# Optimization experiments

Hardware: AMD Instinct MI355X
Metric: run time of the kernel (lower is better)

The kernel has to match this reference:

```python
import jax, jax.numpy as jnp
import numpy as np

# SMPL/STAR kinematic tree: parent of joint i (i = 1..23)
PARENT = np.array([0, 0, 0, 1, 2, 3, 4, 5, 6, 7, 8, 9, 9, 9, 12, 13, 14, 16, 17, 18, 19, 20, 21])
B, V, J, NB = 512, 6890, 24, 10


def _axis_angle_parts(theta):
    # theta: [N,3] axis-angle. Matches STAR: norm of (theta + 1e-8).
    angle = jnp.linalg.norm(theta + 1e-8, axis=1, keepdims=True)  # [N,1]
    normalized = theta / angle
    half = angle * 0.5
    return jnp.cos(half), jnp.sin(half), normalized


def quat_feat(theta):
    c, s, n = _axis_angle_parts(theta)
    return jnp.concatenate([s * n, c - 1.0], axis=1)  # [N,4]


def rodrigues(theta):
    c, s, n = _axis_angle_parts(theta)
    w = c[:, 0]
    xyz = s * n
    x, y, z = xyz[:, 0], xyz[:, 1], xyz[:, 2]
    xx, yy, zz = x * x, y * y, z * z
    wx, wy, wz = w * x, w * y, w * z
    xy, xz, yz = x * y, x * z, y * z
    R = jnp.stack([
        1 - 2 * (yy + zz), 2 * (xy - wz), 2 * (xz + wy),
        2 * (xy + wz), 1 - 2 * (xx + zz), 2 * (yz - wx),
        2 * (xz - wy), 2 * (yz + wx), 1 - 2 * (xx + yy)], axis=-1)
    return R.reshape(-1, 3, 3)


def setup_inputs() -> dict:
    key = jax.random.key(0)
    ks = jax.random.split(key, 8)
    pose = jax.random.normal(ks[0], (B, 72), jnp.float32)
    betas = jax.random.normal(ks[1], (B, NB), jnp.float32)
    trans = jax.random.normal(ks[2], (B, 3), jnp.float32)
    v_template = jax.random.normal(ks[3], (V, 3), jnp.float32)
    shapedirs = jax.random.normal(ks[4], (V * 3, NB), jnp.float32) * 0.01
    posedirs = jax.random.normal(ks[5], (V * 3, 93), jnp.float32) * 0.01
    J_regressor = jax.random.uniform(ks[6], (J, V), jnp.float32)
    J_regressor = J_regressor / jnp.sum(J_regressor, axis=1, keepdims=True)
    weights = jax.random.uniform(ks[7], (V, J), jnp.float32)
    weights = weights / jnp.sum(weights, axis=1, keepdims=True)
    return {"pose": pose, "betas": betas, "trans": trans,
            "v_template": v_template, "shapedirs": shapedirs,
            "posedirs": posedirs, "J_regressor": J_regressor,
            "weights": weights}


def reference(pose, betas, trans, v_template, shapedirs, posedirs, J_regressor, weights):
    b = pose.shape[0]
    # shape blendshapes
    v_shaped = jnp.einsum('dk,bk->bd', shapedirs, betas).reshape(b, V, 3) + v_template[None]
    Jp = jnp.einsum('bik,ji->bjk', v_shaped, J_regressor)
    # pose features: quat feats of joints 1..23 + second beta
    pose_quat = quat_feat(pose.reshape(-1, 3)).reshape(b, -1)   # [b,96]
    pose_feat = jnp.concatenate([pose_quat[:, 4:], betas[:, 1:2]], axis=1)  # [b,93]
    R = rodrigues(pose.reshape(-1, 3)).reshape(b, J, 3, 3)
    # pose blendshapes
    v_posed = v_shaped + jnp.einsum('dk,bk->bd', posedirs, pose_feat).reshape(b, V, 3)
    # relative joint locations
    J_rel = jnp.concatenate([Jp[:, :1], Jp[:, 1:] - Jp[:, PARENT]], axis=1)  # [b,24,3]
    # local transforms [b,24,4,4]
    G_local = jnp.concatenate([R, J_rel[:, :, :, None]], axis=-1)
    pad = jnp.broadcast_to(jnp.array([0., 0., 0., 1.], jnp.float32).reshape(1, 1, 1, 4), (b, J, 1, 4))
    G_local = jnp.concatenate([G_local, pad], axis=2)
    # serial forward kinematics (fixed 24-joint chain)
    Gs = [G_local[:, 0]]
    for i in range(1, J):
        Gs.append(jnp.matmul(Gs[PARENT[i - 1]], G_local[:, i]))
    G = jnp.stack(Gs, axis=1)  # [b,24,4,4]
    posed_joints = G[:, :, :3, 3]
    # remove rest-pose joint transform: translation col -= R_part @ J
    t = jnp.einsum('bjxy,bjy->bjx', G[:, :, :3, :3], Jp)
    G_skin = G.at[:, :, :3, 3].add(-t)
    # skinning: T [b,6890,4,4]
    T = jnp.einsum('vj,bjxy->bvxy', weights, G_skin)
    v_h = jnp.concatenate([v_posed, jnp.ones((b, V, 1), v_posed.dtype)], axis=-1)
    v = jnp.einsum('bvxy,bvy->bvx', T, v_h)[:, :, :3] + trans[:, None, :]
    J_transformed = posed_joints + trans[:, None, :]
    return v, v_posed, v_shaped, J_transformed
```

## Files before the change

### kernel.cpp

```cpp
#include <hip/hip_runtime.h>

constexpr int kB  = 512;
constexpr int kV  = 6890;
constexpr int kJ  = 24;
constexpr int kD  = kV * 3;
constexpr int kNB = 10;
constexpr int kNF = 93;

__global__ __launch_bounds__(256) void kA_js(
    const float* __restrict__ Jreg, const float* __restrict__ shapedirs,
    const float* __restrict__ v_template, float* __restrict__ js,
    float* __restrict__ jt) {
  int jk = blockIdx.x;
  int j = jk / 3, k = jk % 3;
  int tid = threadIdx.x;
  float acc[kNB];
  float accT = 0.f;
#pragma unroll
  for (int nb = 0; nb < kNB; ++nb) acc[nb] = 0.f;
  for (int v = blockIdx.y * 256 + tid; v < kV; v += 1024) {
    float w = Jreg[(size_t)j * kV + v];
    const float* srow = shapedirs + (size_t)(v * 3 + k) * kNB;
    accT += w * v_template[v * 3 + k];
#pragma unroll
    for (int nb = 0; nb < kNB; ++nb) acc[nb] += w * srow[nb];
  }
#pragma unroll
  for (int nb = 0; nb < kNB; ++nb)
#pragma unroll
    for (int off = 32; off > 0; off >>= 1)
      acc[nb] += __shfl_down(acc[nb], off, 64);
#pragma unroll
  for (int off = 32; off > 0; off >>= 1) accT += __shfl_down(accT, off, 64);
  __shared__ float red[4][11];
  int wave = tid >> 6, lane = tid & 63;
  if (lane == 0) {
#pragma unroll
    for (int nb = 0; nb < kNB; ++nb) red[wave][nb] = acc[nb];
    red[wave][10] = accT;
  }
  __syncthreads();
  if (tid == 0) {
#pragma unroll
    for (int nb = 0; nb < kNB; ++nb)
      atomicAdd(&js[jk * kNB + nb],
                red[0][nb] + red[1][nb] + red[2][nb] + red[3][nb]);
    atomicAdd(&jt[jk], red[0][10] + red[1][10] + red[2][10] + red[3][10]);
  }
}

__global__ __launch_bounds__(64) void kC_batch(
    const float* __restrict__ pose, const float* __restrict__ betas,
    const float* __restrict__ trans, const float* __restrict__ js,
    const float* __restrict__ jt, float* __restrict__ pfT,
    float* __restrict__ Gskin, float* __restrict__ out_Jt) {
  const int parent[24] = {-1, 0, 0, 0, 1, 2, 3, 4, 5, 6, 7, 8,
                          9, 9, 9, 12, 13, 14, 16, 17, 18, 19, 20, 21};
  const int depth[24] = {0, 1, 1, 1, 2, 2, 2, 3, 3, 3, 4, 4,
                         4, 4, 4, 5, 5, 5, 6, 6, 7, 7, 8, 8};
  int b = blockIdx.x;
  int j = threadIdx.x;
  __shared__ float G[24][12];
  __shared__ float Jp_s[24][3];
  float R[9];
  if (j < 24) {
    float t0 = pose[b * 72 + 3 * j + 0];
    float t1 = pose[b * 72 + 3 * j + 1];
    float t2 = pose[b * 72 + 3 * j + 2];
    float a0 = t0 + 1e-8f, a1 = t1 + 1e-8f, a2 = t2 + 1e-8f;
    float angle = sqrtf(a0 * a0 + a1 * a1 + a2 * a2);
    float inv = 1.0f / angle;
    float h = 0.5f * angle;
    float c = cosf(h), s = sinf(h);
    float x = s * t0 * inv, y = s * t1 * inv, z = s * t2 * inv, w = c;
    if (j >= 1) {
      int f = 4 * (j - 1);
      pfT[(size_t)(f + 0) * kB + b] = x;
      pfT[(size_t)(f + 1) * kB + b] = y;
      pfT[(size_t)(f + 2) * kB + b] = z;
      pfT[(size_t)(f + 3) * kB + b] = c - 1.0f;
    } else {
      pfT[(size_t)92 * kB + b] = betas[b * kNB + 1];
    }
    float xx = x * x, yy = y * y, zz = z * z;
    float wx = w * x, wy = w * y, wz = w * z;
    float xy = x * y, xz = x * z, yz = y * z;
    R[0] = 1.f - 2.f * (yy + zz); R[1] = 2.f * (xy - wz); R[2] = 2.f * (xz + wy);
    R[3] = 2.f * (xy + wz); R[4] = 1.f - 2.f * (xx + zz); R[5] = 2.f * (yz - wx);
    R[6] = 2.f * (xz - wy); R[7] = 2.f * (yz + wx); R[8] = 1.f - 2.f * (xx + yy);
    float bet[kNB];
#pragma unroll
    for (int nb = 0; nb < kNB; ++nb) bet[nb] = betas[b * kNB + nb];
#pragma unroll
    for (int k = 0; k < 3; ++k) {
      float a = jt[j * 3 + k];
      const float* jr = js + (size_t)(j * 3 + k) * kNB;
#pragma unroll
      for (int nb = 0; nb < kNB; ++nb) a += jr[nb] * bet[nb];
      Jp_s[j][k] = a;
    }
  }
  __syncthreads();
  float tl[3];
  if (j < 24) {
    int p = parent[j];
#pragma unroll
    for (int k = 0; k < 3; ++k)
      tl[k] = (p >= 0) ? (Jp_s[j][k] - Jp_s[p][k]) : Jp_s[j][k];
    if (j == 0) {
#pragma unroll
      for (int r = 0; r < 3; ++r) {
        G[0][r * 4 + 0] = R[r * 3 + 0];
        G[0][r * 4 + 1] = R[r * 3 + 1];
        G[0][r * 4 + 2] = R[r * 3 + 2];
        G[0][r * 4 + 3] = tl[r];
      }
    }
  }
  __syncthreads();
  for (int lev = 1; lev <= 8; ++lev) {
    if (j < 24 && depth[j] == lev) {
      int p = parent[j];
      float nG[12];
#pragma unroll
      for (int r = 0; r < 3; ++r) {
        float g0 = G[p][r * 4 + 0], g1 = G[p][r * 4 + 1];
        float g2 = G[p][r * 4 + 2], g3 = G[p][r * 4 + 3];
        nG[r * 4 + 0] = g0 * R[0] + g1 * R[3] + g2 * R[6];
        nG[r * 4 + 1] = g0 * R[1] + g1 * R[4] + g2 * R[7];
        nG[r * 4 + 2] = g0 * R[2] + g1 * R[5] + g2 * R[8];
        nG[r * 4 + 3] = g0 * tl[0] + g1 * tl[1] + g2 * tl[2] + g3;
      }
#pragma unroll
      for (int e = 0; e < 12; ++e) G[j][e] = nG[e];
    }
    __syncthreads();
  }
  if (j < 24) {
    float tr[3];
#pragma unroll
    for (int k = 0; k < 3; ++k) tr[k] = trans[b * 3 + k];
#pragma unroll
    for (int k = 0; k < 3; ++k)
      out_Jt[b * 72 + j * 3 + k] = G[j][k * 4 + 3] + tr[k];
    float jp0 = Jp_s[j][0], jp1 = Jp_s[j][1], jp2 = Jp_s[j][2];
    float* gs = Gskin + b * 288 + j * 12;
#pragma unroll
    for (int r = 0; r < 3; ++r) {
      float t = G[j][r * 4 + 0] * jp0 + G[j][r * 4 + 1] * jp1 + G[j][r * 4 + 2] * jp2;
      gs[r * 4 + 0] = G[j][r * 4 + 0];
      gs[r * 4 + 1] = G[j][r * 4 + 1];
      gs[r * 4 + 2] = G[j][r * 4 + 2];
      gs[r * 4 + 3] = G[j][r * 4 + 3] - t;
    }
  }
}

__global__ __launch_bounds__(256) void k14_fused(
    const float* __restrict__ shapedirs, const float* __restrict__ posedirs,
    const float* __restrict__ v_template, const float* __restrict__ betas,
    const float* __restrict__ pfT, float* __restrict__ out_vshaped,
    float* __restrict__ out_vposed) {
  int tid = threadIdx.x;
  int d = blockIdx.x * 256 + tid;
  bool active = d < kD;
  int dl = active ? d : (kD - 1);
  float sd[kNB], pd[kNF];
#pragma unroll
  for (int k = 0; k < kNB; ++k) sd[k] = shapedirs[(size_t)dl * kNB + k];
#pragma unroll
  for (int f = 0; f < kNF; ++f) pd[f] = posedirs[(size_t)dl * kNF + f];
  float vt = v_template[dl];
  int b0 = blockIdx.y * 32;
#pragma unroll 1
  for (int bc = 0; bc < 4; ++bc) {
    int bb = b0 + bc * 8;
    float as[8], ap[8];
#pragma unroll
    for (int t = 0; t < 8; ++t) {
      const float* be = betas + (size_t)(bb + t) * kNB;
      float a = vt;
#pragma unroll
      for (int k = 0; k < kNB; ++k) a += sd[k] * be[k];
      as[t] = a;
      ap[t] = a;
    }
#pragma unroll
    for (int f = 0; f < kNF; ++f) {
      float pdf = pd[f];
      const float* q = pfT + (size_t)f * kB + bb;
#pragma unroll
      for (int t = 0; t < 8; ++t) ap[t] += pdf * q[t];
    }
    if (active) {
#pragma unroll
      for (int t = 0; t < 8; ++t) {
        size_t idx = (size_t)(bb + t) * kD + d;
        out_vshaped[idx] = as[t];
        out_vposed[idx] = ap[t];
      }
    }
  }
}

__global__ __launch_bounds__(256) void k5_skin(
    const float* __restrict__ weights, const float* __restrict__ Gskin,
    const float* __restrict__ trans, const float* __restrict__ vposed,
    float* __restrict__ out_v) {
  __shared__ __align__(16) float Gs[8 * 288];
  int tid = threadIdx.x;
  int v = blockIdx.x * 256 + tid;
  bool active = v < kV;
  int vl = active ? v : (kV - 1);
  float w[kJ];
#pragma unroll
  for (int j = 0; j < kJ; ++j) w[j] = weights[(size_t)vl * kJ + j];
  int b0 = blockIdx.y * 8;
  {
    const float* src = Gskin + (size_t)b0 * 288;
#pragma unroll
    for (int i = 0; i < 9; ++i) Gs[i * 256 + tid] = src[i * 256 + tid];
  }
  __syncthreads();
#pragma unroll 1
  for (int bi = 0; bi < 8; ++bi) {
    int b = b0 + bi;
    size_t base = (size_t)b * kD + (size_t)vl * 3;
    float q0 = vposed[base + 0];
    float q1 = vposed[base + 1];
    float q2 = vposed[base + 2];
    float tr0 = trans[b * 3 + 0];
    float tr1 = trans[b * 3 + 1];
    float tr2 = trans[b * 3 + 2];
    const float4* Gt = (const float4*)(Gs + bi * 288);
    float T0 = 0.f, T1 = 0.f, T2 = 0.f, T3 = 0.f;
    float T4 = 0.f, T5 = 0.f, T6 = 0.f, T7 = 0.f;
    float T8 = 0.f, T9 = 0.f, T10 = 0.f, T11 = 0.f;
#pragma unroll 4
    for (int j = 0; j < kJ; ++j) {
      float wj = w[j];
      float4 ga = Gt[j * 3 + 0];
      float4 gb = Gt[j * 3 + 1];
      float4 gc = Gt[j * 3 + 2];
      T0 += wj * ga.x; T1 += wj * ga.y; T2 += wj * ga.z; T3 += wj * ga.w;
      T4 += wj * gb.x; T5 += wj * gb.y; T6 += wj * gb.z; T7 += wj * gb.w;
      T8 += wj * gc.x; T9 += wj * gc.y; T10 += wj * gc.z; T11 += wj * gc.w;
    }
    if (active) {
      out_v[base + 0] = T0 * q0 + T1 * q1 + T2 * q2 + T3 + tr0;
      out_v[base + 1] = T4 * q0 + T5 * q1 + T6 * q2 + T7 + tr1;
      out_v[base + 2] = T8 * q0 + T9 * q1 + T10 * q2 + T11 + tr2;
    }
  }
}

extern "C" void kernel_launch(void* const* d_in, const int* in_sizes, int n_in,
                              void* d_out, int out_size, void* d_ws,
                              size_t ws_size, hipStream_t stream) {
  const float* pose       = (const float*)d_in[0];
  const float* betas      = (const float*)d_in[1];
  const float* trans      = (const float*)d_in[2];
  const float* v_template = (const float*)d_in[3];
  const float* shapedirs  = (const float*)d_in[4];
  const float* posedirs   = (const float*)d_in[5];
  const float* Jreg       = (const float*)d_in[6];
  const float* weights    = (const float*)d_in[7];

  float* out = (float*)d_out;
  float* out_v       = out;
  float* out_vposed  = out + (size_t)kB * kD;
  float* out_vshaped = out + 2 * (size_t)kB * kD;
  float* out_Jt      = out + 3 * (size_t)kB * kD;

  float* wsf   = (float*)d_ws;
  float* pfT   = wsf;
  float* Gskin = pfT + kNF * kB;
  float* js    = Gskin + kB * 288;
  float* jt    = js + 72 * kNB;

  hipMemsetAsync(js, 0, (72 * kNB + 72) * sizeof(float), stream);

  hipLaunchKernelGGL(kA_js, dim3(72, 4), dim3(256), 0, stream, Jreg, shapedirs,
                     v_template, js, jt);
  hipLaunchKernelGGL(kC_batch, dim3(kB), dim3(64), 0, stream, pose, betas,
                     trans, js, jt, pfT, Gskin, out_Jt);
  hipLaunchKernelGGL(k14_fused, dim3((kD + 255) / 256, 16), dim3(256), 0,
                     stream, shapedirs, posedirs, v_template, betas, pfT,
                     out_vshaped, out_vposed);
  hipLaunchKernelGGL(k5_skin, dim3((kV + 255) / 256, 64), dim3(256), 0, stream,
                     weights, Gskin, trans, out_vposed, out_v);
}
```

Measured before the change: 252.2 us.

## Stage pose features and betas in LDS and accumulate 32 batches per thread

The fused shape/pose blendshape kernel now cooperatively loads the block's 93x32 pose-feature tile and 32 beta vectors into shared memory. Previously each thread kept 93 posedirs values in registers and read pfT through global or scalar loads in chunks of 8 batches. Now it streams posedirs once and keeps 32 batch accumulators, reading features as float4 from LDS. This is meant to cut register pressure from the pd array and replace repeated global reads with LDS broadcasts. The cost is a block-wide sync and 32 live accumulators.

```diff
diff --git a/kernel.cpp b/kernel.cpp
--- a/kernel.cpp
+++ b/kernel.cpp
@@ -161,45 +161,62 @@
     const float* __restrict__ v_template, const float* __restrict__ betas,
     const float* __restrict__ pfT, float* __restrict__ out_vshaped,
     float* __restrict__ out_vposed) {
-  int tid = threadIdx.x;
-  int d = blockIdx.x * 256 + tid;
-  bool active = d < kD;
-  int dl = active ? d : (kD - 1);
-  float sd[kNB], pd[kNF];
+  __shared__ __align__(16) float pfs[kNF * 32];
+  __shared__ float bets[32 * 12];
+  const int tid = threadIdx.x;
+  const int d = blockIdx.x * 256 + tid;
+  const bool active = d < kD;
+  const int dl = active ? d : (kD - 1);
+  const int b0 = blockIdx.y * 32;
+
+  for (int i = tid; i < kNF * 32; i += 256) {
+    int f = i >> 5, c = i & 31;
+    pfs[i] = pfT[(size_t)f * kB + b0 + c];
+  }
+  for (int i = tid; i < 32 * kNB; i += 256) {
+    int c = i / kNB, nb = i - c * kNB;
+    bets[c * 12 + nb] = betas[(size_t)(b0 + c) * kNB + nb];
+  }
+
+  float sd[kNB];
 #pragma unroll
   for (int k = 0; k < kNB; ++k) sd[k] = shapedirs[(size_t)dl * kNB + k];
-#pragma unroll
-  for (int f = 0; f < kNF; ++f) pd[f] = posedirs[(size_t)dl * kNF + f];
-  float vt = v_template[dl];
-  int b0 = blockIdx.y * 32;
-#pragma unroll 1
-  for (int bc = 0; bc < 4; ++bc) {
-    int bb = b0 + bc * 8;
-    float as[8], ap[8];
-#pragma unroll
-    for (int t = 0; t < 8; ++t) {
-      const float* be = betas + (size_t)(bb + t) * kNB;
-      float a = vt;
-#pragma unroll
-      for (int k = 0; k < kNB; ++k) a += sd[k] * be[k];
-      as[t] = a;
-      ap[t] = a;
-    }
-#pragma unroll
-    for (int f = 0; f < kNF; ++f) {
-      float pdf = pd[f];
-      const float* q = pfT + (size_t)f * kB + bb;
-#pragma unroll
-      for (int t = 0; t < 8; ++t) ap[t] += pdf * q[t];
-    }
-    if (active) {
-#pragma unroll
-      for (int t = 0; t < 8; ++t) {
-        size_t idx = (size_t)(bb + t) * kD + d;
-        out_vshaped[idx] = as[t];
-        out_vposed[idx] = ap[t];
-      }
-    }
+  const float vt = v_template[dl];
+  const float* prow = posedirs + (size_t)dl * kNF;
+
+  __syncthreads();
+
+  float ap[32];
+#pragma unroll
+  for (int t = 0; t < 32; ++t) {
+    float a = vt;
+#pragma unroll
+    for (int k = 0; k < kNB; ++k) a += sd[k] * bets[t * 12 + k];
+    ap[t] = a;
+    if (active) out_vshaped[(size_t)(b0 + t) * kD + d] = a;
+    if ((t & 7) == 7) __builtin_amdgcn_sched_barrier(0);
+  }
+
+#pragma unroll 2
+  for (int f = 0; f < kNF; ++f) {
+    float pdf = prow[f];
+    const float4* q4 = (const float4*)(pfs + f * 32);
+    float4 qa = q4[0], qb = q4[1], qc = q4[2], qd = q4[3];
+    float4 qe = q4[4], qf = q4[5], qg = q4[6], qh = q4[7];
+    ap[0]  += pdf * qa.x; ap[1]  += pdf * qa.y; ap[2]  += pdf * qa.z; ap[3]  += pdf * qa.w;
+    ap[4]  += pdf * qb.x; ap[5]  += pdf * qb.y; ap[6]  += pdf * qb.z; ap[7]  += pdf * qb.w;
+    ap[8]  += pdf * qc.x; ap[9]  += pdf * qc.y; ap[10] += pdf * qc.z; ap[11] += pdf * qc.w;
+    ap[12] += pdf * qd.x; ap[13] += pdf * qd.y; ap[14] += pdf * qd.z; ap[15] += pdf * qd.w;
+    ap[16] += pdf * qe.x; ap[17] += pdf * qe.y; ap[18] += pdf * qe.z; ap[19] += pdf * qe.w;
+    ap[20] += pdf * qf.x; ap[21] += pdf * qf.y; ap[22] += pdf * qf.z; ap[23] += pdf * qf.w;
+    ap[24] += pdf * qg.x; ap[25] += pdf * qg.y; ap[26] += pdf * qg.z; ap[27] += pdf * qg.w;
+    ap[28] += pdf * qh.x; ap[29] += pdf * qh.y; ap[30] += pdf * qh.z; ap[31] += pdf * qh.w;
+  }
+
+  if (active) {
+#pragma unroll
+    for (int t = 0; t < 32; ++t)
+      out_vposed[(size_t)(b0 + t) * kD + d] = ap[t];
   }
 }
 
```

After: 382.7 us. +51.7%, slower.

## Split pose-blendshape feature reduction across four waves with shared-memory combine

Applied to the files above, without the earlier changes.

The fused blendshape kernel now gives each block 64 output elements, with its four waves each covering a 24-feature slice of the 93 posedirs features. Partial sums are combined through shared memory, and only wave 0 computes the shape blend and writes outputs. The aim is to cut per-thread register use from roughly 103 live floats and to launch four times as many blocks, which should raise occupancy and latency hiding. In exchange it adds two barriers per batch chunk and shared-memory traffic, and each wave reads 24-float strided slices of posedirs rows, which coalesce less well.

```diff
diff --git a/kernel.cpp b/kernel.cpp
--- a/kernel.cpp
+++ b/kernel.cpp
@@ -161,45 +161,76 @@
     const float* __restrict__ v_template, const float* __restrict__ betas,
     const float* __restrict__ pfT, float* __restrict__ out_vshaped,
     float* __restrict__ out_vposed) {
-  int tid = threadIdx.x;
-  int d = blockIdx.x * 256 + tid;
-  bool active = d < kD;
-  int dl = active ? d : (kD - 1);
-  float sd[kNB], pd[kNF];
-#pragma unroll
-  for (int k = 0; k < kNB; ++k) sd[k] = shapedirs[(size_t)dl * kNB + k];
-#pragma unroll
-  for (int f = 0; f < kNF; ++f) pd[f] = posedirs[(size_t)dl * kNF + f];
-  float vt = v_template[dl];
-  int b0 = blockIdx.y * 32;
+  __shared__ float part[3][64][8];
+  const int tid = threadIdx.x;
+  const int dloc = tid & 63;
+  const int d = blockIdx.x * 64 + dloc;
+  const bool active = d < kD;
+  const int dl = active ? d : (kD - 1);
+  const int wv = tid >> 6;
+  const int wb = __builtin_amdgcn_readfirstlane(wv * 24);
+  const int nfc = (kNF - wb) < 24 ? (kNF - wb) : 24;
+  const int b0 = blockIdx.y * 32;
+
+  float pd[24];
+  const float* prow = posedirs + (size_t)dl * kNF + wb;
+#pragma unroll
+  for (int i = 0; i < 24; ++i) pd[i] = (i < nfc) ? prow[i] : 0.f;
+
+  float sd[kNB];
+  float vt = 0.f;
+  if (wv == 0) {
+#pragma unroll
+    for (int k = 0; k < kNB; ++k) sd[k] = shapedirs[(size_t)dl * kNB + k];
+    vt = v_template[dl];
+  }
+
 #pragma unroll 1
   for (int bc = 0; bc < 4; ++bc) {
-    int bb = b0 + bc * 8;
-    float as[8], ap[8];
-#pragma unroll
-    for (int t = 0; t < 8; ++t) {
-      const float* be = betas + (size_t)(bb + t) * kNB;
-      float a = vt;
-#pragma unroll
-      for (int k = 0; k < kNB; ++k) a += sd[k] * be[k];
-      as[t] = a;
-      ap[t] = a;
-    }
-#pragma unroll
-    for (int f = 0; f < kNF; ++f) {
-      float pdf = pd[f];
-      const float* q = pfT + (size_t)f * kB + bb;
-#pragma unroll
-      for (int t = 0; t < 8; ++t) ap[t] += pdf * q[t];
-    }
-    if (active) {
+    const int bb = b0 + bc * 8;
+
+    float ap[8];
+    if (wv == 0) {
 #pragma unroll
       for (int t = 0; t < 8; ++t) {
-        size_t idx = (size_t)(bb + t) * kD + d;
-        out_vshaped[idx] = as[t];
-        out_vposed[idx] = ap[t];
-      }
-    }
+        const float* be = betas + (size_t)(bb + t) * kNB;
+        float a = vt;
+#pragma unroll
+        for (int k = 0; k < kNB; ++k) a += sd[k] * be[k];
+        ap[t] = a;
+        if (active) out_vshaped[(size_t)(bb + t) * kD + d] = a;
+      }
+    } else {
+#pragma unroll
+      for (int t = 0; t < 8; ++t) ap[t] = 0.f;
+    }
+
+#pragma unroll
+    for (int fi = 0; fi < 24; ++fi) {
+      if (wb + fi < kNF) {
+        const float* q = pfT + (size_t)(wb + fi) * kB + bb;
+        float pdf = pd[fi];
+        ap[0] += pdf * q[0]; ap[1] += pdf * q[1];
+        ap[2] += pdf * q[2]; ap[3] += pdf * q[3];
+        ap[4] += pdf * q[4]; ap[5] += pdf * q[5];
+        ap[6] += pdf * q[6]; ap[7] += pdf * q[7];
+      }
+    }
+
+    if (wv != 0) {
+#pragma unroll
+      for (int t = 0; t < 8; ++t) part[wv - 1][dloc][t] = ap[t];
+    }
+    __syncthreads();
+    if (wv == 0 && active) {
+#pragma unroll
+      for (int t = 0; t < 8; ++t) {
+        float s = ap[t] + part[0][dloc][t] + part[1][dloc][t] +
+                  part[2][dloc][t];
+        out_vposed[(size_t)(bb + t) * kD + d] = s;
+      }
+    }
+    __syncthreads();
   }
 }
 
@@ -284,7 +315,7 @@
                      v_template, js, jt);
   hipLaunchKernelGGL(kC_batch, dim3(kB), dim3(64), 0, stream, pose, betas,
                      trans, js, jt, pfT, Gskin, out_Jt);
-  hipLaunchKernelGGL(k14_fused, dim3((kD + 255) / 256, 16), dim3(256), 0,
+  hipLaunchKernelGGL(k14_fused, dim3((kD + 63) / 64, 16), dim3(256), 0,
                      stream, shapedirs, posedirs, v_template, betas, pfT,
                      out_vshaped, out_vposed);
   hipLaunchKernelGGL(k5_skin, dim3((kV + 255) / 256, 64), dim3(256), 0, stream,
```

Measured after the change: 392.7 us. +55.7%, slower.
